# Kernel optimization log

Hardware: AMD Instinct MI355X
Metric: run time of the kernel (lower is better)

The kernel has to match this reference:

```python
import jax, jax.numpy as jnp
import numpy as np

K = 16  # neighbors

def setup_inputs() -> dict:
    key = jax.random.key(0)
    x = jax.random.normal(key, (2, 8192, 64), dtype=jnp.float32)
    return {"x": x}

def reference(x):
    # pairwise squared euclidean distance: ||xi||^2 - 2 xi.xj + ||xj||^2
    b, n, d = x.shape
    x_inner = -2.0 * jnp.einsum('bnd,bmd->bnm', x, x)          # (B,N,N)
    x_sq = jnp.sum(x * x, axis=-1, keepdims=True)               # (B,N,1)
    dist = x_sq + x_inner + jnp.swapaxes(x_sq, 1, 2)            # (B,N,N)
    # torch.topk(-dist, k) -> largest of -dist == k nearest neighbors
    _, nn_idx = jax.lax.top_k(-dist, K)                         # (B,N,K) int32
    center_idx = jnp.broadcast_to(jnp.arange(n, dtype=nn_idx.dtype)[None, :, None], (b, n, K))
    return jnp.stack((nn_idx, center_idx), axis=0)              # (2,B,N,K)
```

## Files before the change

kernel.cpp:

```cpp
#include <hip/hip_runtime.h>
#include <stdint.h>

constexpr int N_    = 8192;
constexpr int D_    = 64;
constexpr int K_    = 16;
constexpr int NQ    = 16384;
constexpr int MS    = 8;
constexpr int CAPB  = 40;

typedef __attribute__((ext_vector_type(8))) short bf16x8;
typedef __attribute__((ext_vector_type(4))) float f32x4;

template<int JN>
__device__ __forceinline__ void topk_insertf(float (&key)[JN], float nk) {
    if (nk < key[JN - 1]) {
        bool c[JN];
#pragma unroll
        for (int j = 0; j < JN; ++j) c[j] = nk < key[j];
#pragma unroll
        for (int j = JN - 1; j >= 1; --j)
            key[j] = c[j - 1] ? key[j - 1] : (c[j] ? nk : key[j]);
        key[0] = c[0] ? nk : key[0];
    }
}

__device__ __forceinline__ unsigned short bf16_rne(float f) {
    uint32_t u = __float_as_uint(f);
    return (unsigned short)((u + 0x7FFFu + ((u >> 16) & 1u)) >> 16);
}

__device__ __forceinline__ void gl_lds16(const void* g, void* l) {
    __builtin_amdgcn_global_load_lds(
        (const __attribute__((address_space(1))) unsigned int*)g,
        (__attribute__((address_space(3))) unsigned int*)l, 16, 0, 0);
}

#define SWZ(r, s) (((r) << 7) + ((((s) ^ ((r) & 7))) << 4))

__global__ void __launch_bounds__(256) split_k(const float* __restrict__ x,
                                               unsigned short* __restrict__ xh,
                                               float* __restrict__ nrm,
                                               float* __restrict__ eres) {
    const int t = blockIdx.x * 256 + (int)threadIdx.x;
    const int row = t >> 4, seg = t & 15;
    const float4 v = reinterpret_cast<const float4*>(x)[t];
    float f[4] = {v.x, v.y, v.z, v.w};
    unsigned short h[4];
    float sq = 0.f, esq = 0.f;
#pragma unroll
    for (int j = 0; j < 4; ++j) {
        sq = fmaf(f[j], f[j], sq);
        h[j] = bf16_rne(f[j]);
        float hf = __uint_as_float((uint32_t)h[j] << 16);
        float r  = f[j] - hf;
        esq = fmaf(r, r, esq);
    }
    sq  += __shfl_xor(sq, 1, 16);  sq  += __shfl_xor(sq, 2, 16);
    sq  += __shfl_xor(sq, 4, 16);  sq  += __shfl_xor(sq, 8, 16);
    esq += __shfl_xor(esq, 1, 16); esq += __shfl_xor(esq, 2, 16);
    esq += __shfl_xor(esq, 4, 16); esq += __shfl_xor(esq, 8, 16);
    if (seg == 0) { nrm[row] = sq; eres[row] = sqrtf(esq); }
    ushort4 hv = {h[0], h[1], h[2], h[3]};
    reinterpret_cast<ushort4*>(xh)[t] = hv;
}

__global__ void __launch_bounds__(256) red_k(const float* __restrict__ nrm,
                                             const float* __restrict__ eres,
                                             float* __restrict__ EH) {
    __shared__ float mbuf[8];
    const int b = (int)blockIdx.x, tid = (int)threadIdx.x;
    float mn = 0.f, me = 0.f;
    for (int i = tid; i < N_; i += 256) {
        mn = fmaxf(mn, nrm[b * N_ + i]);
        me = fmaxf(me, eres[b * N_ + i]);
    }
#pragma unroll
    for (int s = 1; s < 64; s <<= 1) {
        mn = fmaxf(mn, __shfl_xor(mn, s, 64));
        me = fmaxf(me, __shfl_xor(me, s, 64));
    }
    const int w = tid >> 6;
    if ((tid & 63) == 0) { mbuf[w * 2] = mn; mbuf[w * 2 + 1] = me; }
    __syncthreads();
    if (tid == 0) {
        for (int i = 1; i < 4; ++i) {
            mn = fmaxf(mn, mbuf[i * 2]); me = fmaxf(me, mbuf[i * 2 + 1]);
        }
        EH[b * 2]     = sqrtf(mn) * 1.0002f + 1e-6f;
        EH[b * 2 + 1] = me * 1.0002f + 1e-7f;
    }
}

__global__ void __launch_bounds__(256, 4) tau_p(const unsigned short* __restrict__ xh,
                                                const float* __restrict__ nrm,
                                                float* __restrict__ part) {
    __shared__ alignas(16) unsigned short Bd[2][64 * 64];
    __shared__ alignas(16) float nrmS[512];
    const int tid = (int)threadIdx.x;
    const int bid = (int)blockIdx.x;
    const int qb  = bid >> 2, sh = bid & 3;
    const int q0g = qb * 64;
    const int b   = q0g >> 13;
    const int q0l = q0g & (N_ - 1);
    const int s0  = sh * 512;
    const unsigned short* __restrict__ xhb = xh + (size_t)b * N_ * D_;
    const float* __restrict__ nb = nrm + b * N_;
    const int w = tid >> 6, lane = tid & 63;
    const int wq = w >> 1, wm = w & 1;
    const int l15 = lane & 15, quad = lane >> 4;

    bf16x8 Af[2][2];
#pragma unroll
    for (int half = 0; half < 2; ++half) {
        const int ko = (half * 4 + quad) << 4;
#pragma unroll
        for (int tm = 0; tm < 2; ++tm) {
            const int r = q0l + wq * 32 + tm * 16 + l15;
            Af[half][tm] = *(const bf16x8*)((const char*)(xhb + (size_t)r * D_) + ko);
        }
    }
    {
#pragma unroll
        for (int k = 0; k < 2; ++k) {
            int u = k * 256 + tid, r = u >> 3, sg = (u & 7) ^ (r & 7);
            gl_lds16((const char*)(xhb + (size_t)(s0 + r) * D_) + (sg << 4),
                     (char*)Bd[0] + (k << 12) + (w << 10));
        }
    }
    *(float2*)(nrmS + tid * 2) = *(const float2*)(nb + s0 + tid * 2);

    float lad[8];
#pragma unroll
    for (int j = 0; j < 8; ++j) lad[j] = __builtin_inff();
    __syncthreads();

    for (int mc = 0; mc < 8; ++mc) {
        const int cur = mc & 1;
        if (mc < 7) {
            const int m0n = s0 + (mc + 1) * 64;
#pragma unroll
            for (int k = 0; k < 2; ++k) {
                int u = k * 256 + tid, r = u >> 3, sg = (u & 7) ^ (r & 7);
                gl_lds16((const char*)(xhb + (size_t)(m0n + r) * D_) + (sg << 4),
                         (char*)Bd[1 - cur] + (k << 12) + (w << 10));
            }
        }
        f32x4 acc[2][2] = {};
#pragma unroll
        for (int half = 0; half < 2; ++half) {
            const int seg = half * 4 + quad;
            bf16x8 bf[2];
#pragma unroll
            for (int tn = 0; tn < 2; ++tn)
                bf[tn] = *(const bf16x8*)((const char*)Bd[cur] + SWZ(wm * 32 + tn * 16 + l15, seg));
#pragma unroll
            for (int tm = 0; tm < 2; ++tm)
#pragma unroll
                for (int tn = 0; tn < 2; ++tn)
                    acc[tm][tn] = __builtin_amdgcn_mfma_f32_16x16x32_bf16(Af[half][tm], bf[tn], acc[tm][tn], 0, 0, 0);
        }
#pragma unroll
        for (int tn = 0; tn < 2; ++tn) {
            const float nm = nrmS[mc * 64 + wm * 32 + tn * 16 + l15];
#pragma unroll
            for (int tm = 0; tm < 2; ++tm)
#pragma unroll
                for (int reg = 0; reg < 4; ++reg)
                    lad[tm * 4 + reg] = fminf(lad[tm * 4 + reg],
                                              fmaf(-2.f, acc[tm][tn][reg], nm));
        }
        __syncthreads();
    }
#pragma unroll
    for (int tm = 0; tm < 2; ++tm)
#pragma unroll
        for (int reg = 0; reg < 4; ++reg) {
            const int q = q0g + wq * 32 + tm * 16 + quad * 4 + reg;
            part[(size_t)q * 128 + sh * 32 + wm * 16 + l15] = lad[tm * 4 + reg];
        }
}

__global__ void __launch_bounds__(64) tau_m(const float* __restrict__ part,
                                            const float* __restrict__ nrm,
                                            const float* __restrict__ eres,
                                            const float* __restrict__ EH,
                                            float* __restrict__ tau) {
    const int q = blockIdx.x * 64 + (int)threadIdx.x;
    const int b = q >> 13;
    const float4* p = reinterpret_cast<const float4*>(part + (size_t)q * 128);
    float key[K_];
#pragma unroll
    for (int j = 0; j < K_; ++j) key[j] = __builtin_inff();
    for (int i = 0; i < 32; ++i) {
        float4 v = p[i];
        topk_insertf<K_>(key, v.x); topk_insertf<K_>(key, v.y);
        topk_insertf<K_>(key, v.z); topk_insertf<K_>(key, v.w);
    }
    const float Nmax = EH[b * 2], Emax = EH[b * 2 + 1];
    const float H = Nmax + Emax;
    const float nq = sqrtf(nrm[q]) * 1.0001f, eq = eres[q];
    tau[q] = key[15] + 4.f * (nq * Emax + eq * H) + 6e-3f;
}

__global__ void __launch_bounds__(256, 3) filter_k(const unsigned short* __restrict__ xh,
                                                   const float* __restrict__ nrm,
                                                   const float* __restrict__ tau,
                                                   unsigned short* __restrict__ cnt_pb,
                                                   unsigned short* __restrict__ buf2) {
    __shared__ alignas(16) unsigned short A[128 * 64];
    __shared__ alignas(16) unsigned short Bd[2][64 * 64];
    __shared__ alignas(16) float nrmS[1024];
    __shared__ unsigned short lists[128 * CAPB];
    __shared__ unsigned int cntL[128];
    const int tid = (int)threadIdx.x;
    const int bid = (int)blockIdx.x;
    const int b  = bid >> 9;
    const int qt = (bid >> 3) & 63;
    const int ms = bid & 7;
    const int q0 = qt * 128;
    const unsigned short* __restrict__ xhb = xh + (size_t)b * N_ * D_;
    const float* __restrict__ nb = nrm + b * N_;
    const int w = tid >> 6, lane = tid & 63;
    const int wq = w >> 1, wm = w & 1;
    const int l15 = lane & 15, quad = lane >> 4;

#pragma unroll
    for (int k = 0; k < 4; ++k) {
        int u = k * 256 + tid, r = u >> 3, sg = (u & 7) ^ (r & 7);
        gl_lds16((const char*)(xhb + (size_t)(q0 + r) * D_) + (sg << 4),
                 (char*)A + (k << 12) + (w << 10));
    }
    {
        const int m0 = ms * 1024;
#pragma unroll
        for (int k = 0; k < 2; ++k) {
            int u = k * 256 + tid, r = u >> 3, sg = (u & 7) ^ (r & 7);
            gl_lds16((const char*)(xhb + (size_t)(m0 + r) * D_) + (sg << 4),
                     (char*)Bd[0] + (k << 12) + (w << 10));
        }
    }
    *(float4*)(nrmS + tid * 4) = *(const float4*)(nb + ms * 1024 + tid * 4);
    if (tid < 128) cntL[tid] = 0;
    f32x4 t4v[4];
#pragma unroll
    for (int tm = 0; tm < 4; ++tm)
        t4v[tm] = *(const f32x4*)(tau + (b << 13) + q0 + wq * 64 + tm * 16 + quad * 4);
    __syncthreads();

    bf16x8 Af[2][4];
#pragma unroll
    for (int half = 0; half < 2; ++half) {
        const int seg = half * 4 + quad;
#pragma unroll
        for (int tm = 0; tm < 4; ++tm)
            Af[half][tm] = *(const bf16x8*)((const char*)A + SWZ(wq * 64 + tm * 16 + l15, seg));
    }

    for (int mc = 0; mc < 16; ++mc) {
        const int cur = mc & 1;
        if (mc < 15) {
            const int m0n = ms * 1024 + (mc + 1) * 64;
#pragma unroll
            for (int k = 0; k < 2; ++k) {
                int u = k * 256 + tid, r = u >> 3, sg = (u & 7) ^ (r & 7);
                gl_lds16((const char*)(xhb + (size_t)(m0n + r) * D_) + (sg << 4),
                         (char*)Bd[1 - cur] + (k << 12) + (w << 10));
            }
        }
        f32x4 acc[4][2] = {};
#pragma unroll
        for (int half = 0; half < 2; ++half) {
            const int seg = half * 4 + quad;
            bf16x8 bf[2];
#pragma unroll
            for (int tn = 0; tn < 2; ++tn)
                bf[tn] = *(const bf16x8*)((const char*)Bd[cur] + SWZ(wm * 32 + tn * 16 + l15, seg));
#pragma unroll
            for (int tm = 0; tm < 4; ++tm)
#pragma unroll
                for (int tn = 0; tn < 2; ++tn)
                    acc[tm][tn] = __builtin_amdgcn_mfma_f32_16x16x32_bf16(Af[half][tm], bf[tn], acc[tm][tn], 0, 0, 0);
        }
#pragma unroll
        for (int tn = 0; tn < 2; ++tn) {
            const int mloc = wm * 32 + tn * 16 + l15;
            const float nm = nrmS[mc * 64 + mloc];
            const unsigned short mid = (unsigned short)(ms * 1024 + mc * 64 + mloc);
#pragma unroll
            for (int tm = 0; tm < 4; ++tm)
#pragma unroll
                for (int reg = 0; reg < 4; ++reg) {
                    float keyf = fmaf(-2.f, acc[tm][tn][reg], nm);
                    if (keyf <= t4v[tm][reg]) {
                        int ql = wq * 64 + tm * 16 + quad * 4 + reg;
                        unsigned pos = atomicAdd(&cntL[ql], 1u);
                        if (pos < CAPB) lists[ql * CAPB + pos] = mid;
                    }
                }
        }
        __syncthreads();
    }
    if (tid < 128) {
        const int q = (b << 13) + q0 + tid;
        unsigned cn = cntL[tid]; cn = cn < CAPB ? cn : CAPB;
        cnt_pb[(size_t)q * MS + ms] = (unsigned short)cn;
        unsigned short* dst = buf2 + ((size_t)q * MS + ms) * CAPB;
        for (unsigned i = 0; i < cn; ++i) dst[i] = lists[tid * CAPB + i];
    }
}

__global__ void __launch_bounds__(256) rerank_k(const float* __restrict__ x,
                                                const unsigned short* __restrict__ cnt_pb,
                                                const unsigned short* __restrict__ buf2,
                                                int* __restrict__ out) {
    __shared__ float Qs[4 * 64];
    __shared__ unsigned short ids[4 * MS * CAPB];
    const int tid = (int)threadIdx.x;
    const int w = tid >> 6, lane = tid & 63;
    const int q = blockIdx.x * 4 + w;
    const int b = q >> 13, n = q & (N_ - 1);
    const float* __restrict__ xb = x + (size_t)b * N_ * D_;
    Qs[w * 64 + lane] = xb[(size_t)n * D_ + lane];

    int off[MS + 1]; off[0] = 0;
#pragma unroll
    for (int ms = 0; ms < MS; ++ms) {
        int c = (int)cnt_pb[(size_t)q * MS + ms]; c = c < CAPB ? c : CAPB;
        off[ms + 1] = off[ms] + c;
    }
    const int total = off[MS];
    for (int idx = lane; idx < total; idx += 64) {
        int ms = 0;
#pragma unroll
        for (int t = 1; t < MS; ++t) ms += (idx >= off[t]) ? 1 : 0;
        ids[(w * MS) * CAPB + idx] = buf2[((size_t)q * MS + ms) * CAPB + (idx - off[ms])];
    }
    __syncthreads();

    unsigned long long v = ~0ull;
    int consumed = 0;
    bool first = true;
    while (first || consumed < total) {
        const int myIdx = first ? lane : consumed + lane - 16;
        const bool take = (first || lane >= 16) && myIdx < total;
        unsigned long long nk = ~0ull;
        if (take) {
            const int id = (int)ids[(w * MS) * CAPB + myIdx];
            const float* __restrict__ crow = xb + (size_t)id * D_;
            double a0 = 0.0, a1 = 0.0, a2 = 0.0, a3 = 0.0;
#pragma unroll
            for (int j = 0; j < 16; ++j) {
                const float4 c  = *(const float4*)(crow + j * 4);
                const float4 qv = *(const float4*)(Qs + w * 64 + j * 4);
                double d0 = (double)qv.x - (double)c.x; a0 = fma(d0, d0, a0);
                double d1 = (double)qv.y - (double)c.y; a1 = fma(d1, d1, a1);
                double d2 = (double)qv.z - (double)c.z; a2 = fma(d2, d2, a2);
                double d3 = (double)qv.w - (double)c.w; a3 = fma(d3, d3, a3);
            }
            double s = (a0 + a1) + (a2 + a3);
            nk = ((unsigned long long)__double_as_longlong(s) & ~0x1FFFull) | (unsigned)id;
        }
        if (first || lane >= 16) v = nk;
#pragma unroll
        for (int k = 2; k <= 64; k <<= 1)
#pragma unroll
            for (int j = k >> 1; j > 0; j >>= 1) {
                unsigned long long o = __shfl_xor(v, j, 64);
                const bool keepmin = (((lane & k) == 0) == ((lane & j) == 0));
                unsigned long long mn = v < o ? v : o;
                unsigned long long mx = v < o ? o : v;
                v = keepmin ? mn : mx;
            }
        consumed += first ? 64 : 48;
        first = false;
    }
    if (lane < K_) {
        out[(size_t)q * K_ + lane]                   = (int)(v & 0x1FFFull);
        out[(size_t)NQ * K_ + (size_t)q * K_ + lane] = n;
    }
}

extern "C" void kernel_launch(void* const* d_in, const int* in_sizes, int n_in,
                              void* d_out, int out_size, void* d_ws, size_t ws_size,
                              hipStream_t stream) {
    const float* x = (const float*)d_in[0];
    int* out = (int*)d_out;
    char* ws = (char*)d_ws;
    float*          nrm    = (float*)ws;
    float*          tau    = (float*)(ws + (64 << 10));
    float*          eres   = (float*)(ws + (128 << 10));
    float*          EH     = (float*)(ws + (192 << 10));
    unsigned short* cnt_pb = (unsigned short*)(ws + (256 << 10));
    unsigned short* xh     = (unsigned short*)(ws + (1 << 20));
    unsigned short* buf2   = (unsigned short*)(ws + (5 << 20));
    float*          part   = (float*)(ws + (5 << 20));

    hipLaunchKernelGGL(split_k,  dim3(1024), dim3(256), 0, stream, x, xh, nrm, eres);
    hipLaunchKernelGGL(red_k,    dim3(2),    dim3(256), 0, stream, nrm, eres, EH);
    hipLaunchKernelGGL(tau_p,    dim3(1024), dim3(256), 0, stream, xh, nrm, part);
    hipLaunchKernelGGL(tau_m,    dim3(256),  dim3(64),  0, stream, part, nrm, eres, EH, tau);
    hipLaunchKernelGGL(filter_k, dim3(1024), dim3(256), 0, stream, xh, nrm, tau, cnt_pb, buf2);
    hipLaunchKernelGGL(rerank_k, dim3(4096), dim3(256), 0, stream, x, cnt_pb, buf2, out);
}
```

Before: 249.3 us.

## Load MFMA operands directly from global memory instead of staging through LDS

Both the tau_p and filter_k GEMM-like kernels stop staging A and B tiles into swizzled LDS with async global_load_lds double buffering. Each wave now loads its bf16 fragments straight from global memory into registers, and the per-iteration barriers are removed. tau_p also doubles its query tile to 128 rows per block, which halves its grid, and filter_k's occupancy hint is raised to 4. The aim is to cut LDS traffic and synchronization and to raise occupancy, at the cost of redundant global/L2 reads across waves and no explicit prefetch overlap.

```diff
diff --git a/kernel.cpp b/kernel.cpp
--- a/kernel.cpp
+++ b/kernel.cpp
@@ -28,14 +28,6 @@
     uint32_t u = __float_as_uint(f);
     return (unsigned short)((u + 0x7FFFu + ((u >> 16) & 1u)) >> 16);
 }
-
-__device__ __forceinline__ void gl_lds16(const void* g, void* l) {
-    __builtin_amdgcn_global_load_lds(
-        (const __attribute__((address_space(1))) unsigned int*)g,
-        (__attribute__((address_space(3))) unsigned int*)l, 16, 0, 0);
-}
-
-#define SWZ(r, s) (((r) << 7) + ((((s) ^ ((r) & 7))) << 4))
 
 __global__ void __launch_bounds__(256) split_k(const float* __restrict__ x,
                                                unsigned short* __restrict__ xh,
@@ -94,12 +86,11 @@
 __global__ void __launch_bounds__(256, 4) tau_p(const unsigned short* __restrict__ xh,
                                                 const float* __restrict__ nrm,
                                                 float* __restrict__ part) {
-    __shared__ alignas(16) unsigned short Bd[2][64 * 64];
     __shared__ alignas(16) float nrmS[512];
     const int tid = (int)threadIdx.x;
     const int bid = (int)blockIdx.x;
-    const int qb  = bid >> 2, sh = bid & 3;
-    const int q0g = qb * 64;
+    const int qt  = bid >> 2, sh = bid & 3;
+    const int q0g = qt * 128;
     const int b   = q0g >> 13;
     const int q0l = q0g & (N_ - 1);
     const int s0  = sh * 512;
@@ -109,73 +100,55 @@
     const int wq = w >> 1, wm = w & 1;
     const int l15 = lane & 15, quad = lane >> 4;
 
-    bf16x8 Af[2][2];
+    if (tid < 128) *(float4*)(nrmS + tid * 4) = *(const float4*)(nb + s0 + tid * 4);
+
+    bf16x8 Af[2][4];
 #pragma unroll
     for (int half = 0; half < 2; ++half) {
-        const int ko = (half * 4 + quad) << 4;
-#pragma unroll
-        for (int tm = 0; tm < 2; ++tm) {
-            const int r = q0l + wq * 32 + tm * 16 + l15;
-            Af[half][tm] = *(const bf16x8*)((const char*)(xhb + (size_t)r * D_) + ko);
-        }
-    }
-    {
-#pragma unroll
-        for (int k = 0; k < 2; ++k) {
-            int u = k * 256 + tid, r = u >> 3, sg = (u & 7) ^ (r & 7);
-            gl_lds16((const char*)(xhb + (size_t)(s0 + r) * D_) + (sg << 4),
-                     (char*)Bd[0] + (k << 12) + (w << 10));
-        }
-    }
-    *(float2*)(nrmS + tid * 2) = *(const float2*)(nb + s0 + tid * 2);
-
-    float lad[8];
-#pragma unroll
-    for (int j = 0; j < 8; ++j) lad[j] = __builtin_inff();
+        const int eo = (half * 4 + quad) * 8;
+#pragma unroll
+        for (int tm = 0; tm < 4; ++tm)
+            Af[half][tm] = *(const bf16x8*)(xhb + (size_t)(q0l + wq * 64 + tm * 16 + l15) * D_ + eo);
+    }
+    float lad[16];
+#pragma unroll
+    for (int j = 0; j < 16; ++j) lad[j] = __builtin_inff();
     __syncthreads();
 
     for (int mc = 0; mc < 8; ++mc) {
-        const int cur = mc & 1;
-        if (mc < 7) {
-            const int m0n = s0 + (mc + 1) * 64;
-#pragma unroll
-            for (int k = 0; k < 2; ++k) {
-                int u = k * 256 + tid, r = u >> 3, sg = (u & 7) ^ (r & 7);
-                gl_lds16((const char*)(xhb + (size_t)(m0n + r) * D_) + (sg << 4),
-                         (char*)Bd[1 - cur] + (k << 12) + (w << 10));
-            }
-        }
-        f32x4 acc[2][2] = {};
+        const unsigned short* Bbase = xhb + (size_t)(s0 + mc * 64) * D_;
+        bf16x8 Bf[2][2];
 #pragma unroll
         for (int half = 0; half < 2; ++half) {
-            const int seg = half * 4 + quad;
-            bf16x8 bf[2];
+            const int eo = (half * 4 + quad) * 8;
 #pragma unroll
             for (int tn = 0; tn < 2; ++tn)
-                bf[tn] = *(const bf16x8*)((const char*)Bd[cur] + SWZ(wm * 32 + tn * 16 + l15, seg));
-#pragma unroll
-            for (int tm = 0; tm < 2; ++tm)
+                Bf[half][tn] = *(const bf16x8*)(Bbase + (size_t)(wm * 32 + tn * 16 + l15) * D_ + eo);
+        }
+        f32x4 acc[4][2] = {};
+#pragma unroll
+        for (int half = 0; half < 2; ++half)
+#pragma unroll
+            for (int tm = 0; tm < 4; ++tm)
 #pragma unroll
                 for (int tn = 0; tn < 2; ++tn)
-                    acc[tm][tn] = __builtin_amdgcn_mfma_f32_16x16x32_bf16(Af[half][tm], bf[tn], acc[tm][tn], 0, 0, 0);
-        }
+                    acc[tm][tn] = __builtin_amdgcn_mfma_f32_16x16x32_bf16(Af[half][tm], Bf[half][tn], acc[tm][tn], 0, 0, 0);
 #pragma unroll
         for (int tn = 0; tn < 2; ++tn) {
             const float nm = nrmS[mc * 64 + wm * 32 + tn * 16 + l15];
 #pragma unroll
-            for (int tm = 0; tm < 2; ++tm)
+            for (int tm = 0; tm < 4; ++tm)
 #pragma unroll
                 for (int reg = 0; reg < 4; ++reg)
                     lad[tm * 4 + reg] = fminf(lad[tm * 4 + reg],
                                               fmaf(-2.f, acc[tm][tn][reg], nm));
         }
-        __syncthreads();
-    }
-#pragma unroll
-    for (int tm = 0; tm < 2; ++tm)
+    }
+#pragma unroll
+    for (int tm = 0; tm < 4; ++tm)
 #pragma unroll
         for (int reg = 0; reg < 4; ++reg) {
-            const int q = q0g + wq * 32 + tm * 16 + quad * 4 + reg;
+            const int q = q0g + wq * 64 + tm * 16 + quad * 4 + reg;
             part[(size_t)q * 128 + sh * 32 + wm * 16 + l15] = lad[tm * 4 + reg];
         }
 }
@@ -202,13 +175,11 @@
     tau[q] = key[15] + 4.f * (nq * Emax + eq * H) + 6e-3f;
 }
 
-__global__ void __launch_bounds__(256, 3) filter_k(const unsigned short* __restrict__ xh,
+__global__ void __launch_bounds__(256, 4) filter_k(const unsigned short* __restrict__ xh,
                                                    const float* __restrict__ nrm,
                                                    const float* __restrict__ tau,
                                                    unsigned short* __restrict__ cnt_pb,
                                                    unsigned short* __restrict__ buf2) {
-    __shared__ alignas(16) unsigned short A[128 * 64];
-    __shared__ alignas(16) unsigned short Bd[2][64 * 64];
     __shared__ alignas(16) float nrmS[1024];
     __shared__ unsigned short lists[128 * CAPB];
     __shared__ unsigned int cntL[128];
@@ -224,68 +195,46 @@
     const int wq = w >> 1, wm = w & 1;
     const int l15 = lane & 15, quad = lane >> 4;
 
-#pragma unroll
-    for (int k = 0; k < 4; ++k) {
-        int u = k * 256 + tid, r = u >> 3, sg = (u & 7) ^ (r & 7);
-        gl_lds16((const char*)(xhb + (size_t)(q0 + r) * D_) + (sg << 4),
-                 (char*)A + (k << 12) + (w << 10));
-    }
-    {
-        const int m0 = ms * 1024;
-#pragma unroll
-        for (int k = 0; k < 2; ++k) {
-            int u = k * 256 + tid, r = u >> 3, sg = (u & 7) ^ (r & 7);
-            gl_lds16((const char*)(xhb + (size_t)(m0 + r) * D_) + (sg << 4),
-                     (char*)Bd[0] + (k << 12) + (w << 10));
-        }
-    }
     *(float4*)(nrmS + tid * 4) = *(const float4*)(nb + ms * 1024 + tid * 4);
     if (tid < 128) cntL[tid] = 0;
+
+    bf16x8 Af[2][4];
+#pragma unroll
+    for (int half = 0; half < 2; ++half) {
+        const int eo = (half * 4 + quad) * 8;
+#pragma unroll
+        for (int tm = 0; tm < 4; ++tm)
+            Af[half][tm] = *(const bf16x8*)(xhb + (size_t)(q0 + wq * 64 + tm * 16 + l15) * D_ + eo);
+    }
     f32x4 t4v[4];
 #pragma unroll
     for (int tm = 0; tm < 4; ++tm)
         t4v[tm] = *(const f32x4*)(tau + (b << 13) + q0 + wq * 64 + tm * 16 + quad * 4);
     __syncthreads();
 
-    bf16x8 Af[2][4];
-#pragma unroll
-    for (int half = 0; half < 2; ++half) {
-        const int seg = half * 4 + quad;
-#pragma unroll
-        for (int tm = 0; tm < 4; ++tm)
-            Af[half][tm] = *(const bf16x8*)((const char*)A + SWZ(wq * 64 + tm * 16 + l15, seg));
-    }
-
     for (int mc = 0; mc < 16; ++mc) {
-        const int cur = mc & 1;
-        if (mc < 15) {
-            const int m0n = ms * 1024 + (mc + 1) * 64;
-#pragma unroll
-            for (int k = 0; k < 2; ++k) {
-                int u = k * 256 + tid, r = u >> 3, sg = (u & 7) ^ (r & 7);
-                gl_lds16((const char*)(xhb + (size_t)(m0n + r) * D_) + (sg << 4),
-                         (char*)Bd[1 - cur] + (k << 12) + (w << 10));
-            }
+        const unsigned short* Bbase = xhb + (size_t)(ms * 1024 + mc * 64) * D_;
+        bf16x8 Bf[2][2];
+#pragma unroll
+        for (int half = 0; half < 2; ++half) {
+            const int eo = (half * 4 + quad) * 8;
+#pragma unroll
+            for (int tn = 0; tn < 2; ++tn)
+                Bf[half][tn] = *(const bf16x8*)(Bbase + (size_t)(wm * 32 + tn * 16 + l15) * D_ + eo);
         }
         f32x4 acc[4][2] = {};
 #pragma unroll
-        for (int half = 0; half < 2; ++half) {
-            const int seg = half * 4 + quad;
-            bf16x8 bf[2];
-#pragma unroll
-            for (int tn = 0; tn < 2; ++tn)
-                bf[tn] = *(const bf16x8*)((const char*)Bd[cur] + SWZ(wm * 32 + tn * 16 + l15, seg));
+        for (int half = 0; half < 2; ++half)
 #pragma unroll
             for (int tm = 0; tm < 4; ++tm)
 #pragma unroll
                 for (int tn = 0; tn < 2; ++tn)
-                    acc[tm][tn] = __builtin_amdgcn_mfma_f32_16x16x32_bf16(Af[half][tm], bf[tn], acc[tm][tn], 0, 0, 0);
-        }
+                    acc[tm][tn] = __builtin_amdgcn_mfma_f32_16x16x32_bf16(Af[half][tm], Bf[half][tn], acc[tm][tn], 0, 0, 0);
 #pragma unroll
         for (int tn = 0; tn < 2; ++tn) {
-            const int mloc = wm * 32 + tn * 16 + l15;
-            const float nm = nrmS[mc * 64 + mloc];
-            const unsigned short mid = (unsigned short)(ms * 1024 + mc * 64 + mloc);
+            const int mloc = mc * 64 + wm * 32 + tn * 16 + l15;
+            const float nm = nrmS[mloc];
+            const unsigned short mid = (unsigned short)(ms * 1024 + mloc);
 #pragma unroll
             for (int tm = 0; tm < 4; ++tm)
 #pragma unroll
@@ -298,8 +247,8 @@
                     }
                 }
         }
-        __syncthreads();
-    }
+    }
+    __syncthreads();
     if (tid < 128) {
         const int q = (b << 13) + q0 + tid;
         unsigned cn = cntL[tid]; cn = cn < CAPB ? cn : CAPB;
@@ -397,7 +346,7 @@
 
     hipLaunchKernelGGL(split_k,  dim3(1024), dim3(256), 0, stream, x, xh, nrm, eres);
     hipLaunchKernelGGL(red_k,    dim3(2),    dim3(256), 0, stream, nrm, eres, EH);
-    hipLaunchKernelGGL(tau_p,    dim3(1024), dim3(256), 0, stream, xh, nrm, part);
+    hipLaunchKernelGGL(tau_p,    dim3(512),  dim3(256), 0, stream, xh, nrm, part);
     hipLaunchKernelGGL(tau_m,    dim3(256),  dim3(64),  0, stream, part, nrm, eres, EH, tau);
     hipLaunchKernelGGL(filter_k, dim3(1024), dim3(256), 0, stream, xh, nrm, tau, cnt_pb, buf2);
     hipLaunchKernelGGL(rerank_k, dim3(4096), dim3(256), 0, stream, x, cnt_pb, buf2, out);
```

New measurement: 208.5 us. 1.2x faster.
